# Performance work log

Measured on AMD Instinct MI355X. Metric: run time of the kernel, lower is better.

The kernel has to match this reference:

```python
import jax, jax.numpy as jnp
import numpy as np

LN_EPS = 1e-5

def layer_norm(x, w, b):
    m = jnp.mean(x, axis=-1, keepdims=True)
    v = jnp.mean((x - m) ** 2, axis=-1, keepdims=True)
    return (x - m) * jax.lax.rsqrt(v + LN_EPS) * w + b

def setup_inputs() -> dict:
    key = jax.random.key(0)
    ks = jax.random.split(key, 10)
    B, N, L = 32, 576, 100
    low, high = 1024, 1536
    inp = {
        "vit_feat": jax.random.normal(ks[0], (B, N, low), dtype=jnp.float32),
        "box_feat": jax.random.normal(ks[1], (B, L, high), dtype=jnp.float32),
        "lengths": jax.random.randint(ks[2], (B,), 0, L, dtype=jnp.int64),
        # query projector: LayerNorm(low) + Linear(low, low)
        "q_ln_w": jnp.ones((low,), jnp.float32),
        "q_ln_b": jnp.zeros((low,), jnp.float32),
        "q_w": jax.random.normal(ks[3], (low, low), dtype=jnp.float32) * 0.02,
        "q_b": jnp.zeros((low,), jnp.float32),
        # key projector: LayerNorm(high) + Linear(high, low)
        "k_ln_w": jnp.ones((high,), jnp.float32),
        "k_ln_b": jnp.zeros((high,), jnp.float32),
        "k_w": jax.random.normal(ks[4], (high, low), dtype=jnp.float32) * 0.02,
        "k_b": jnp.zeros((low,), jnp.float32),
        # value projector: LayerNorm(high) + Linear(high, low)
        "v_ln_w": jnp.ones((high,), jnp.float32),
        "v_ln_b": jnp.zeros((high,), jnp.float32),
        "v_w": jax.random.normal(ks[5], (high, low), dtype=jnp.float32) * 0.02,
        "v_b": jnp.zeros((low,), jnp.float32),
    }
    return inp

def reference(vit_feat, box_feat, lengths,
              q_ln_w, q_ln_b, q_w, q_b,
              k_ln_w, k_ln_b, k_w, k_b,
              v_ln_w, v_ln_b, v_w, v_b):
    B, L = box_feat.shape[0], box_feat.shape[1]
    # padding mask, same as the original per-row copy loop
    mask = jnp.arange(L)[None, :] < lengths[:, None]          # [B, L] bool
    q = layer_norm(vit_feat, q_ln_w, q_ln_b) @ q_w + q_b      # [B, N, low]
    k = layer_norm(box_feat, k_ln_w, k_ln_b) @ k_w + k_b      # [B, L, low]
    v = layer_norm(box_feat, v_ln_w, v_ln_b) @ v_w + v_b      # [B, L, low]
    scale = 1.0 / jnp.sqrt(jnp.asarray(k.shape[-1], q.dtype))
    att = jnp.einsum('bnd,bld->bnl', q, k * scale)            # [B, N, L]
    att = jnp.where(mask[:, None, :], att, -jnp.inf)
    att = jnp.nan_to_num(att)  # -inf -> finite min, matching torch nan_to_num
    att = jax.nn.softmax(att, axis=-1)
    out = jnp.einsum('bnl,bld->bnd', att, v)                  # [B, N, low]
    return vit_feat + out
```

## Files before the change

### kernel.cpp

```cpp
#include <hip/hip_runtime.h>
#include <stdint.h>

typedef __attribute__((ext_vector_type(8))) short short8;
typedef __attribute__((ext_vector_type(4))) float f32x4;

#define NEG_FLT_MAX (-3.402823466e38f)

__device__ __forceinline__ unsigned short f2bf(float f) {
  uint32_t u = __float_as_uint(f);
  uint32_t r = (u + 0x7fffu + ((u >> 16) & 1u)) >> 16;
  return (unsigned short)r;
}

__device__ __forceinline__ void gload16(const void* g, void* l) {
  __builtin_amdgcn_global_load_lds(
      (const __attribute__((address_space(1))) uint32_t*)g,
      (__attribute__((address_space(3))) uint32_t*)l, 16, 0, 0);
}

__device__ __forceinline__ void ln_vit_row(
    int row, const float* __restrict__ x, const float* __restrict__ w,
    const float* __restrict__ b, unsigned short* __restrict__ out, float* red) {
  const int t = threadIdx.x;
  const float4 v = ((const float4*)(x + (size_t)row * 1024))[t];
  float s = v.x + v.y + v.z + v.w;
  float ss = v.x * v.x + v.y * v.y + v.z * v.z + v.w * v.w;
#pragma unroll
  for (int off = 32; off > 0; off >>= 1) {
    s += __shfl_xor(s, off);
    ss += __shfl_xor(ss, off);
  }
  if ((t & 63) == 0) { red[(t >> 6) * 2] = s; red[(t >> 6) * 2 + 1] = ss; }
  __syncthreads();
  if (t == 0) {
    float a = 0.f, bb = 0.f;
    for (int i = 0; i < 4; i++) { a += red[i * 2]; bb += red[i * 2 + 1]; }
    red[0] = a; red[1] = bb;
  }
  __syncthreads();
  s = red[0]; ss = red[1];
  const float m = s * (1.f / 1024.f);
  const float var = ss * (1.f / 1024.f) - m * m;
  const float rstd = rsqrtf(var + 1e-5f);
  const float4 w4 = ((const float4*)w)[t];
  const float4 b4 = ((const float4*)b)[t];
  ushort4 o;
  o.x = f2bf((v.x - m) * rstd * w4.x + b4.x);
  o.y = f2bf((v.y - m) * rstd * w4.y + b4.y);
  o.z = f2bf((v.z - m) * rstd * w4.z + b4.z);
  o.w = f2bf((v.w - m) * rstd * w4.w + b4.w);
  ((ushort4*)(out + (size_t)row * 1024))[t] = o;
}

__device__ __forceinline__ void prep_body(
    int bid, const float* __restrict__ qw, const float* __restrict__ kw,
    const float* __restrict__ vw, const float* __restrict__ qb,
    const float* __restrict__ kb, float scale,
    unsigned short* __restrict__ qwb, unsigned short* __restrict__ kwb,
    unsigned short* __restrict__ vwt,
    float* __restrict__ bias3, float* __restrict__ w4, float* __restrict__ c4,
    float* tile ) {
  const int t = threadIdx.x;
  if (bid < 2560) {
    const int idx = bid * 256 + t;
    const int QG = 1024 * 1024 / 4;
    if (idx < QG) {
      float4 v = ((const float4*)qw)[idx];
      ushort4 o;
      o.x = f2bf(v.x); o.y = f2bf(v.y); o.z = f2bf(v.z); o.w = f2bf(v.w);
      ((ushort4*)qwb)[idx] = o;
    } else {
      const int j = idx - QG;
      float4 v = ((const float4*)kw)[j];
      ushort4 o;
      o.x = f2bf(v.x * scale); o.y = f2bf(v.y * scale);
      o.z = f2bf(v.z * scale); o.w = f2bf(v.w * scale);
      ((ushort4*)kwb)[j] = o;
    }
  } else if (bid < 4096) {
    const int j = bid - 2560;
    const int c0 = (j & 31) * 32, r0 = (j >> 5) * 32;
    const int tx = t & 31, ty = t >> 5;
#pragma unroll
    for (int i = ty; i < 32; i += 8)
      tile[i * 33 + tx] = vw[(size_t)(r0 + i) * 1024 + (c0 + tx)];
    __syncthreads();
#pragma unroll
    for (int i = ty; i < 32; i += 8)
      vwt[(size_t)(c0 + i) * 1536 + (r0 + tx)] = f2bf(tile[tx * 33 + i]);
  } else {
    const int idx = bid - 4096;
    const int wv = t >> 6, l = t & 63;
    float s = 0.f;
    if (idx < 256) {
      const int i = idx * 4 + wv;
      const float* row = qw + (size_t)i * 1024;
#pragma unroll
      for (int s0 = 0; s0 < 1024; s0 += 256) {
        float4 a = *(const float4*)(row + s0 + l * 4);
        float4 b = *(const float4*)(kb + s0 + l * 4);
        s += a.x * b.x + a.y * b.y + a.z * b.z + a.w * b.w;
      }
#pragma unroll
      for (int off = 32; off; off >>= 1) s += __shfl_xor(s, off);
      if (l == 0) bias3[i] = s * scale;
    } else if (idx < 640) {
      const int j = (idx - 256) * 4 + wv;
      const float* row = kw + (size_t)j * 1024;
#pragma unroll
      for (int s0 = 0; s0 < 1024; s0 += 256) {
        float4 a = *(const float4*)(row + s0 + l * 4);
        float4 b = *(const float4*)(qb + s0 + l * 4);
        s += a.x * b.x + a.y * b.y + a.z * b.z + a.w * b.w;
      }
#pragma unroll
      for (int off = 32; off; off >>= 1) s += __shfl_xor(s, off);
      if (l == 0) w4[j] = s * scale;
    } else if (wv == 0) {
#pragma unroll
      for (int s0 = 0; s0 < 1024; s0 += 256) {
        float4 a = *(const float4*)(qb + s0 + l * 4);
        float4 b = *(const float4*)(kb + s0 + l * 4);
        s += a.x * b.x + a.y * b.y + a.z * b.z + a.w * b.w;
      }
#pragma unroll
      for (int off = 32; off; off >>= 1) s += __shfl_xor(s, off);
      if (l == 0) *c4 = s * scale;
    }
  }
}

__global__ __launch_bounds__(256) void prep_kernel(
    const float* __restrict__ qw, const float* __restrict__ kw,
    const float* __restrict__ vw, const float* __restrict__ qb,
    const float* __restrict__ kb, float scale,
    unsigned short* __restrict__ qwb, unsigned short* __restrict__ kwb,
    unsigned short* __restrict__ vwt,
    float* __restrict__ bias3, float* __restrict__ w4, float* __restrict__ c4) {
  __shared__ float tile[32 * 33];
  prep_body(blockIdx.x, qw, kw, vw, qb, kb, scale, qwb, kwb, vwt,
            bias3, w4, c4, tile);
}

__global__ __launch_bounds__(256) void prepln_kernel(
    const float* __restrict__ qw, const float* __restrict__ kw,
    const float* __restrict__ vw, const float* __restrict__ qb,
    const float* __restrict__ kb, float scale,
    unsigned short* __restrict__ qwb, unsigned short* __restrict__ kwb,
    unsigned short* __restrict__ vwt,
    float* __restrict__ bias3, float* __restrict__ w4, float* __restrict__ c4,
    const float* __restrict__ vit, const float* __restrict__ qlnw,
    const float* __restrict__ qlnb, unsigned short* __restrict__ qn) {
  __shared__ float tile[32 * 33];
  __shared__ float red[8];
  const int bid = blockIdx.x;
  if (bid < 4737) {
    prep_body(bid, qw, kw, vw, qb, kb, scale, qwb, kwb, vwt,
              bias3, w4, c4, tile);
  } else {
    ln_vit_row(bid - 4737, vit, qlnw, qlnb, qn, red);
  }
}

__device__ __forceinline__ void gemm_core64(
    const unsigned short* __restrict__ A, int lda, int rowmaxA, int tm0,
    const unsigned short* __restrict__ Bt, int ldb, int rowmaxB, int tn0,
    int K, unsigned short* As, unsigned short* Bs, f32x4 acc[4][4]) {
  const int tid = threadIdx.x;
  const int w = tid >> 6, l = tid & 63;
  const int wr = w >> 1, wc = w & 1;
  const int srow = (w << 4) + (l >> 2);
  const int scol = (l & 3) << 3;
  int ra0 = tm0 + srow;      if (ra0 > rowmaxA) ra0 = rowmaxA;
  int ra1 = tm0 + srow + 64; if (ra1 > rowmaxA) ra1 = rowmaxA;
  int rb0 = tn0 + srow;      if (rb0 > rowmaxB) rb0 = rowmaxB;
  int rb1 = tn0 + srow + 64; if (rb1 > rowmaxB) rb1 = rowmaxB;
  const unsigned short* pa0 = A + (size_t)ra0 * lda + scol;
  const unsigned short* pa1 = A + (size_t)ra1 * lda + scol;
  const unsigned short* pb0 = Bt + (size_t)rb0 * ldb + scol;
  const unsigned short* pb1 = Bt + (size_t)rb1 * ldb + scol;
  unsigned short* la0 = As + (w << 4) * 32;
  unsigned short* la1 = As + ((w << 4) + 64) * 32;
  unsigned short* lb0 = Bs + (w << 4) * 32;
  unsigned short* lb1 = Bs + ((w << 4) + 64) * 32;
  const int foff = ((l & 15) << 5) + ((l >> 4) << 3);
  const unsigned short* fa = As + (wr << 6) * 32 + foff;
  const unsigned short* fb = Bs + (wc << 6) * 32 + foff;
#pragma unroll
  for (int i = 0; i < 4; i++)
#pragma unroll
    for (int j = 0; j < 4; j++) acc[i][j] = (f32x4)0.0f;
  for (int k0 = 0; k0 < K; k0 += 64) {
    gload16(pa0 + k0, la0);
    gload16(pa1 + k0, la1);
    gload16(pb0 + k0, lb0);
    gload16(pb1 + k0, lb1);
    gload16(pa0 + k0 + 32, la0 + 4096);
    gload16(pa1 + k0 + 32, la1 + 4096);
    gload16(pb0 + k0 + 32, lb0 + 4096);
    gload16(pb1 + k0 + 32, lb1 + 4096);
    __syncthreads();
    {
      short8 a[4], b[4];
#pragma unroll
      for (int i = 0; i < 4; i++) a[i] = *(const short8*)(fa + i * 512);
#pragma unroll
      for (int j = 0; j < 4; j++) b[j] = *(const short8*)(fb + j * 512);
#pragma unroll
      for (int i = 0; i < 4; i++)
#pragma unroll
        for (int j = 0; j < 4; j++)
          acc[i][j] = __builtin_amdgcn_mfma_f32_16x16x32_bf16(a[i], b[j], acc[i][j], 0, 0, 0);
    }
    {
      short8 a[4], b[4];
#pragma unroll
      for (int i = 0; i < 4; i++) a[i] = *(const short8*)(fa + 4096 + i * 512);
#pragma unroll
      for (int j = 0; j < 4; j++) b[j] = *(const short8*)(fb + 4096 + j * 512);
#pragma unroll
      for (int i = 0; i < 4; i++)
#pragma unroll
        for (int j = 0; j < 4; j++)
          acc[i][j] = __builtin_amdgcn_mfma_f32_16x16x32_bf16(a[i], b[j], acc[i][j], 0, 0, 0);
    }
    __syncthreads();
  }
}

__device__ __forceinline__ void gemm_core_db(
    const unsigned short* __restrict__ A, int lda, int rowmaxA, int tm0,
    const unsigned short* __restrict__ Bt, int ldb, int rowmaxB, int tn0,
    int K, unsigned short* As, unsigned short* Bs, f32x4 acc[4][4]) {
  const int tid = threadIdx.x;
  const int w = tid >> 6, l = tid & 63;
  const int wr = w >> 1, wc = w & 1;
  const int srow = (w << 4) + (l >> 2);
  const int scol = (l & 3) << 3;
  int ra0 = tm0 + srow;      if (ra0 > rowmaxA) ra0 = rowmaxA;
  int ra1 = tm0 + srow + 64; if (ra1 > rowmaxA) ra1 = rowmaxA;
  int rb0 = tn0 + srow;      if (rb0 > rowmaxB) rb0 = rowmaxB;
  int rb1 = tn0 + srow + 64; if (rb1 > rowmaxB) rb1 = rowmaxB;
  const unsigned short* pa0 = A + (size_t)ra0 * lda + scol;
  const unsigned short* pa1 = A + (size_t)ra1 * lda + scol;
  const unsigned short* pb0 = Bt + (size_t)rb0 * ldb + scol;
  const unsigned short* pb1 = Bt + (size_t)rb1 * ldb + scol;
  unsigned short* la0 = As + (w << 4) * 32;
  unsigned short* la1 = As + ((w << 4) + 64) * 32;
  unsigned short* lb0 = Bs + (w << 4) * 32;
  unsigned short* lb1 = Bs + ((w << 4) + 64) * 32;
  const int faoff = (wr << 6) * 32 + ((l & 15) << 5) + ((l >> 4) << 3);
  const int fboff = (wc << 6) * 32 + ((l & 15) << 5) + ((l >> 4) << 3);
#pragma unroll
  for (int i = 0; i < 4; i++)
#pragma unroll
    for (int j = 0; j < 4; j++) acc[i][j] = (f32x4)0.0f;

#define STAGE8(k0, bo) do {                                                  \
    gload16(pa0 + (k0), la0 + (bo));                                         \
    gload16(pa1 + (k0), la1 + (bo));                                         \
    gload16(pb0 + (k0), lb0 + (bo));                                         \
    gload16(pb1 + (k0), lb1 + (bo));                                         \
    gload16(pa0 + (k0) + 32, la0 + (bo) + 4096);                             \
    gload16(pa1 + (k0) + 32, la1 + (bo) + 4096);                             \
    gload16(pb0 + (k0) + 32, lb0 + (bo) + 4096);                             \
    gload16(pb1 + (k0) + 32, lb1 + (bo) + 4096);                             \
  } while (0)

  STAGE8(0, 0);
  __syncthreads();
  int p = 0;
  for (int k0 = 0; k0 < K; k0 += 64) {
    if (k0 + 64 < K) STAGE8(k0 + 64, (p ^ 1) * 8192);
    const unsigned short* fa = As + p * 8192 + faoff;
    const unsigned short* fb = Bs + p * 8192 + fboff;
    {
      short8 a[4], b[4];
#pragma unroll
      for (int i = 0; i < 4; i++) a[i] = *(const short8*)(fa + i * 512);
#pragma unroll
      for (int j = 0; j < 4; j++) b[j] = *(const short8*)(fb + j * 512);
#pragma unroll
      for (int i = 0; i < 4; i++)
#pragma unroll
        for (int j = 0; j < 4; j++)
          acc[i][j] = __builtin_amdgcn_mfma_f32_16x16x32_bf16(a[i], b[j], acc[i][j], 0, 0, 0);
    }
    {
      short8 a[4], b[4];
#pragma unroll
      for (int i = 0; i < 4; i++) a[i] = *(const short8*)(fa + 4096 + i * 512);
#pragma unroll
      for (int j = 0; j < 4; j++) b[j] = *(const short8*)(fb + 4096 + j * 512);
#pragma unroll
      for (int i = 0; i < 4; i++)
#pragma unroll
        for (int j = 0; j < 4; j++)
          acc[i][j] = __builtin_amdgcn_mfma_f32_16x16x32_bf16(a[i], b[j], acc[i][j], 0, 0, 0);
    }
    __syncthreads();
    p ^= 1;
  }
#undef STAGE8
}

__global__ __launch_bounds__(256) void mid_kernel(
    const float* __restrict__ box,
    const float* __restrict__ klnw, const float* __restrict__ klnb,
    const float* __restrict__ vlnw, const float* __restrict__ vlnb,
    const unsigned short* __restrict__ qwb, const unsigned short* __restrict__ kwb,
    const float* __restrict__ w4v, const float* __restrict__ c4,
    unsigned short* __restrict__ kn, unsigned short* __restrict__ vn,
    unsigned short* __restrict__ W3, float* __restrict__ qbk) {
  __shared__ float red[8];
  __shared__ float redq[4];
  __shared__ unsigned short As[128 * 64];
  __shared__ unsigned short Bs[128 * 64];
  const int t = threadIdx.x;
  if (blockIdx.x < 3200) {
    const int row = blockIdx.x;
    const float4* xr = (const float4*)(box + (size_t)row * 1536);
    const float4 a = xr[t];
    float4 c = make_float4(0.f, 0.f, 0.f, 0.f);
    if (t < 128) c = xr[256 + t];
    float s = a.x + a.y + a.z + a.w + c.x + c.y + c.z + c.w;
    float ss = a.x * a.x + a.y * a.y + a.z * a.z + a.w * a.w +
               c.x * c.x + c.y * c.y + c.z * c.z + c.w * c.w;
#pragma unroll
    for (int off = 32; off > 0; off >>= 1) {
      s += __shfl_xor(s, off);
      ss += __shfl_xor(ss, off);
    }
    if ((t & 63) == 0) { red[(t >> 6) * 2] = s; red[(t >> 6) * 2 + 1] = ss; }
    __syncthreads();
    if (t == 0) {
      float aa = 0.f, bb = 0.f;
      for (int i = 0; i < 4; i++) { aa += red[i * 2]; bb += red[i * 2 + 1]; }
      red[0] = aa; red[1] = bb;
    }
    __syncthreads();
    s = red[0]; ss = red[1];
    const float m = s * (1.f / 1536.f);
    const float var = ss * (1.f / 1536.f) - m * m;
    const float rstd = rsqrtf(var + 1e-5f);
    float qd;
    {
      const float4 w4 = ((const float4*)klnw)[t];
      const float4 b4 = ((const float4*)klnb)[t];
      const float k0v = (a.x - m) * rstd * w4.x + b4.x;
      const float k1v = (a.y - m) * rstd * w4.y + b4.y;
      const float k2v = (a.z - m) * rstd * w4.z + b4.z;
      const float k3v = (a.w - m) * rstd * w4.w + b4.w;
      ushort4 o;
      o.x = f2bf(k0v); o.y = f2bf(k1v); o.z = f2bf(k2v); o.w = f2bf(k3v);
      ((ushort4*)(kn + (size_t)row * 1536))[t] = o;
      const float4 wq = ((const float4*)w4v)[t];
      qd = k0v * wq.x + k1v * wq.y + k2v * wq.z + k3v * wq.w;
      const float4 w4vv = ((const float4*)vlnw)[t];
      const float4 b4vv = ((const float4*)vlnb)[t];
      o.x = f2bf((a.x - m) * rstd * w4vv.x + b4vv.x);
      o.y = f2bf((a.y - m) * rstd * w4vv.y + b4vv.y);
      o.z = f2bf((a.z - m) * rstd * w4vv.z + b4vv.z);
      o.w = f2bf((a.w - m) * rstd * w4vv.w + b4vv.w);
      ((ushort4*)(vn + (size_t)row * 1536))[t] = o;
    }
    if (t < 128) {
      const int t2 = 256 + t;
      const float4 w4 = ((const float4*)klnw)[t2];
      const float4 b4 = ((const float4*)klnb)[t2];
      const float k0v = (c.x - m) * rstd * w4.x + b4.x;
      const float k1v = (c.y - m) * rstd * w4.y + b4.y;
      const float k2v = (c.z - m) * rstd * w4.z + b4.z;
      const float k3v = (c.w - m) * rstd * w4.w + b4.w;
      ushort4 o;
      o.x = f2bf(k0v); o.y = f2bf(k1v); o.z = f2bf(k2v); o.w = f2bf(k3v);
      ((ushort4*)(kn + (size_t)row * 1536))[t2] = o;
      const float4 wq = ((const float4*)w4v)[t2];
      qd += k0v * wq.x + k1v * wq.y + k2v * wq.z + k3v * wq.w;
      const float4 w4vv = ((const float4*)vlnw)[t2];
      const float4 b4vv = ((const float4*)vlnb)[t2];
      o.x = f2bf((c.x - m) * rstd * w4vv.x + b4vv.x);
      o.y = f2bf((c.y - m) * rstd * w4vv.y + b4vv.y);
      o.z = f2bf((c.z - m) * rstd * w4vv.z + b4vv.z);
      o.w = f2bf((c.w - m) * rstd * w4vv.w + b4vv.w);
      ((ushort4*)(vn + (size_t)row * 1536))[t2] = o;
    }
#pragma unroll
    for (int off = 32; off; off >>= 1) qd += __shfl_xor(qd, off);
    if ((t & 63) == 0) redq[t >> 6] = qd;
    __syncthreads();
    if (t == 0) qbk[row] = redq[0] + redq[1] + redq[2] + redq[3] + c4[0];
  } else {
    const int j = blockIdx.x - 3200;
    const int tm0 = (j & 7) * 128, tn0 = (j >> 3) * 128;
    f32x4 acc[4][4];
    gemm_core64(qwb, 1024, 1023, tm0, kwb, 1024, 1535, tn0, 1024, As, Bs, acc);
    const int w = t >> 6, l = t & 63;
    const int wr = w >> 1, wc = w & 1;
#pragma unroll
    for (int i = 0; i < 4; i++) {
      const int row0 = tm0 + wr * 64 + i * 16 + (l >> 4) * 4;
#pragma unroll
      for (int jj = 0; jj < 4; jj++) {
        const int col = tn0 + wc * 64 + jj * 16 + (l & 15);
#pragma unroll
        for (int r = 0; r < 4; r++)
          W3[(size_t)(row0 + r) * 1536 + col] = f2bf(acc[i][jj][r]);
      }
    }
  }
}

__global__ __launch_bounds__(256) void gemm_kv_kernel(
    const unsigned short* __restrict__ kn, const unsigned short* __restrict__ vn,
    const unsigned short* __restrict__ W3, const unsigned short* __restrict__ vwt,
    const float* __restrict__ bias3, const float* __restrict__ vb,
    unsigned short* __restrict__ kq, unsigned short* __restrict__ vT) {
  extern __shared__ unsigned short lds[];
  unsigned short* As = lds;
  unsigned short* Bs = lds + 16384;
  const int id = blockIdx.x;
  const int sw = (id & 7) * 50 + (id >> 3);
  const int z = sw / 200;
  const int rem = sw - z * 200;
  const int tm0 = (rem % 25) * 128, tn0 = (rem / 25) * 128;
  const unsigned short* A = z ? vn : kn;
  const unsigned short* Bt = z ? vwt : W3;
  const float* bias = z ? vb : bias3;
  f32x4 acc[4][4];
  gemm_core_db(A, 1536, 3199, tm0, Bt, 1536, 1023, tn0, 1536, As, Bs, acc);
  const int tid = threadIdx.x;
  const int w = tid >> 6, l = tid & 63;
  const int wr = w >> 1, wc = w & 1;
#pragma unroll
  for (int i = 0; i < 4; i++) {
    const int row0 = tm0 + wr * 64 + i * 16 + (l >> 4) * 4;
#pragma unroll
    for (int j = 0; j < 4; j++) {
      const int col = tn0 + wc * 64 + j * 16 + (l & 15);
      const float bv = bias[col];
#pragma unroll
      for (int r = 0; r < 4; r++) {
        const int row = row0 + r;
        const float val = acc[i][j][r] + bv;
        if (!z) {
          kq[(size_t)row * 1024 + col] = f2bf(val);
        } else {
          const int bb = row / 100;
          const int ll = row - bb * 100;
          vT[((size_t)bb * 1024 + col) * 128 + ll] = f2bf(val);
        }
      }
    }
  }
}

__global__ __launch_bounds__(256) void ln_vit_kernel(
    const float* __restrict__ x, const float* __restrict__ w,
    const float* __restrict__ b, unsigned short* __restrict__ out) {
  __shared__ float red[8];
  ln_vit_row(blockIdx.x, x, w, b, out, red);
}

__global__ __launch_bounds__(256) void attfused_kernel(
    const unsigned short* __restrict__ qn, const unsigned short* __restrict__ kq,
    const unsigned short* __restrict__ vT, const float* __restrict__ qbk,
    const int* __restrict__ lengths, const float* __restrict__ vit,
    float* __restrict__ out) {
  __shared__ __align__(16) char smem[45824];
  float* Smat = (float*)smem;
  float* invr = (float*)(smem + 28672);
  float* qb_l = (float*)(smem + 28800);
  const int PB = 20480, BV = 29440;

  const int id = blockIdx.x;
  const int swz = (id & 7) * 72 + (id >> 3);
  const int b = swz / 18;
  const int tm0 = (swz - b * 18) * 32;
  const int t = threadIdx.x;
  const int w = t >> 6, l = t & 63;
  const int lo = l & 15, hi = l >> 4;
  if (t < 128) qb_l[t] = (t < 100) ? qbk[b * 100 + t] : 0.f;

  const unsigned short* A = qn + (size_t)b * 576 * 1024;
  const unsigned short* B = kq + (size_t)b * 100 * 1024;
  const int ar = (t & 127) >> 2, ah = t >> 7, ac = (t & 3) << 3;
  const unsigned short* paA = A + (size_t)(tm0 + ar) * 1024 + ah * 32 + ac;
  const unsigned short* pbB[4];
#pragma unroll
  for (int i = 0; i < 4; i++) {
    int rb = (i & 1) * 64 + (t >> 2); if (rb > 99) rb = 99;
    pbB[i] = B + (size_t)rb * 1024 + (i >> 1) * 32 + ((t & 3) << 3);
  }
  const int cw = w << 5;

  f32x4 acc[2][2];
#pragma unroll
  for (int i = 0; i < 2; i++) { acc[i][0] = (f32x4)0.0f; acc[i][1] = (f32x4)0.0f; }

  for (int k0 = 0; k0 < 1024; k0 += 64) {
    gload16(paA + k0, smem + w * 1024);
#pragma unroll
    for (int i = 0; i < 4; i++)
      gload16(pbB[i] + k0, smem + 4096 + i * 4096 + w * 1024);
    __syncthreads();
#pragma unroll
    for (int half = 0; half < 2; half++) {
      short8 a[2], bb[2];
#pragma unroll
      for (int i = 0; i < 2; i++)
        a[i] = *(const short8*)(smem + half * 2048 + (i * 16 + lo) * 64 + hi * 16);
#pragma unroll
      for (int j = 0; j < 2; j++)
        bb[j] = *(const short8*)(smem + 4096 + half * 8192 + (cw + j * 16 + lo) * 64 + hi * 16);
#pragma unroll
      for (int i = 0; i < 2; i++)
#pragma unroll
        for (int j = 0; j < 2; j++)
          acc[i][j] = __builtin_amdgcn_mfma_f32_16x16x32_bf16(a[i], bb[j], acc[i][j], 0, 0, 0);
    }
    __syncthreads();
  }

#pragma unroll
  for (int i = 0; i < 2; i++) {
    const int r0 = i * 16 + hi * 4;
#pragma unroll
    for (int j = 0; j < 2; j++) {
      const int c = cw + j * 16 + lo;
      const float qb = qb_l[c];
#pragma unroll
      for (int rr = 0; rr < 4; rr++) Smat[c * 36 + r0 + rr] = acc[i][j][rr] + qb;
    }
  }
  __syncthreads();

  const int r = t >> 3, g = t & 7;
  const int len = lengths[b];
  float mx = NEG_FLT_MAX;
#pragma unroll
  for (int i = 0; i < 13; i++) {
    const int ll = g * 13 + i;
    if (ll < 100) {
      const float v = (ll < len) ? Smat[ll * 36 + r] : NEG_FLT_MAX;
      mx = fmaxf(mx, v);
    }
  }
  mx = fmaxf(mx, __shfl_xor(mx, 1));
  mx = fmaxf(mx, __shfl_xor(mx, 2));
  mx = fmaxf(mx, __shfl_xor(mx, 4));
  float sum = 0.f;
#pragma unroll
  for (int i = 0; i < 13; i++) {
    const int ll = g * 13 + i;
    if (ll < 100) {
      const float v = (ll < len) ? Smat[ll * 36 + r] : NEG_FLT_MAX;
      const float e = __expf(v - mx);
      Smat[ll * 36 + r] = e;
      sum += e;
    }
  }
  sum += __shfl_xor(sum, 1);
  sum += __shfl_xor(sum, 2);
  sum += __shfl_xor(sum, 4);
  if (g == 0) invr[r] = 1.f / sum;
  __syncthreads();

  {
    const float inv = invr[r];
#pragma unroll
    for (int jj = 0; jj < 4; jj++) {
      const int c0 = g * 16 + jj * 4;
      ushort4 o;
      o.x = (c0 + 0 < 100) ? f2bf(Smat[(c0 + 0) * 36 + r] * inv) : (unsigned short)0;
      o.y = (c0 + 1 < 100) ? f2bf(Smat[(c0 + 1) * 36 + r] * inv) : (unsigned short)0;
      o.z = (c0 + 2 < 100) ? f2bf(Smat[(c0 + 2) * 36 + r] * inv) : (unsigned short)0;
      o.w = (c0 + 3 < 100) ? f2bf(Smat[(c0 + 3) * 36 + r] * inv) : (unsigned short)0;
      const int phys = (r * 256 + g * 32 + jj * 8) ^ ((r & 7) << 4);
      *(ushort4*)(smem + PB + phys) = o;
    }
  }
  __syncthreads();

  const unsigned short* vTb = vT + (size_t)b * 131072;
  const float* vitb = vit + ((size_t)b * 576 + tm0) * 1024;
  float* outb = out + ((size_t)b * 576 + tm0) * 1024;
  const int sBcol = ((t & 15) ^ ((t >> 4) & 7)) << 3;
  for (int nt = 0; nt < 16; ++nt) {
#pragma unroll
    for (int i = 0; i < 4; i++) {
      const int vrow = nt * 64 + i * 16 + (t >> 4);
      gload16(vTb + (size_t)vrow * 128 + sBcol, smem + BV + i * 4096 + w * 1024);
    }
    __syncthreads();
    f32x4 acc2[2];
    acc2[0] = (f32x4)0.0f; acc2[1] = (f32x4)0.0f;
#pragma unroll
    for (int ks = 0; ks < 4; ks++) {
      short8 av[2], bv;
#pragma unroll
      for (int i = 0; i < 2; i++) {
        const int m = i * 16 + lo;
        av[i] = *(const short8*)(smem + PB + ((m * 256 + ks * 64 + hi * 16) ^ ((m & 7) << 4)));
      }
      const int n = (w << 4) + lo;
      bv = *(const short8*)(smem + BV + ((n * 256 + ks * 64 + hi * 16) ^ ((n & 7) << 4)));
      acc2[0] = __builtin_amdgcn_mfma_f32_16x16x32_bf16(av[0], bv, acc2[0], 0, 0, 0);
      acc2[1] = __builtin_amdgcn_mfma_f32_16x16x32_bf16(av[1], bv, acc2[1], 0, 0, 0);
    }
#pragma unroll
    for (int i = 0; i < 2; i++) {
      const int col = (w << 4) + lo;
#pragma unroll
      for (int rr = 0; rr < 4; rr++) {
        const int row = i * 16 + hi * 4 + rr;
        *(float*)(smem + ((row * 256 + col * 4) ^ ((row & 7) << 4))) = acc2[i][rr];
      }
    }
    __syncthreads();
#pragma unroll
    for (int m = 0; m < 2; m++) {
      const int row = m * 16 + (t >> 4);
      const int colb = (t & 15) * 4;
      float4 e = *(const float4*)(smem + ((row * 256 + colb * 4) ^ ((row & 7) << 4)));
      const size_t gidx = (size_t)row * 1024 + nt * 64 + colb;
      float4 vv = *(const float4*)(vitb + gidx);
      e.x += vv.x; e.y += vv.y; e.z += vv.z; e.w += vv.w;
      *(float4*)(outb + gidx) = e;
    }
    __syncthreads();
  }
}

extern "C" void kernel_launch(void* const* d_in, const int* in_sizes, int n_in,
                              void* d_out, int out_size, void* d_ws, size_t ws_size,
                              hipStream_t stream) {
  const float* vit = (const float*)d_in[0];
  const float* box = (const float*)d_in[1];
  const int* lengths = (const int*)d_in[2];
  const float* q_ln_w = (const float*)d_in[3];
  const float* q_ln_b = (const float*)d_in[4];
  const float* q_w = (const float*)d_in[5];
  const float* q_b = (const float*)d_in[6];
  const float* k_ln_w = (const float*)d_in[7];
  const float* k_ln_b = (const float*)d_in[8];
  const float* k_w = (const float*)d_in[9];
  const float* k_b = (const float*)d_in[10];
  const float* v_ln_w = (const float*)d_in[11];
  const float* v_ln_b = (const float*)d_in[12];
  const float* v_w = (const float*)d_in[13];
  const float* v_b = (const float*)d_in[14];
  float* out = (float*)d_out;
  char* ws = (char*)d_ws;

  unsigned short* kn    = (unsigned short*)(ws + 0);
  unsigned short* vn    = (unsigned short*)(ws + 9830400);
  unsigned short* v_wt  = (unsigned short*)(ws + 19660800);
  unsigned short* qwb   = (unsigned short*)(ws + 22806528);
  unsigned short* kwb   = (unsigned short*)(ws + 24903680);
  unsigned short* W3    = (unsigned short*)(ws + 28049408);
  float*          bias3 = (float*)(ws + 31195136);
  float*          w4    = (float*)(ws + 31199232);
  float*          c4    = (float*)(ws + 31207424);
  float*          qbk   = (float*)(ws + 37748736);
  unsigned short* kq    = (unsigned short*)(ws + 37761536);
  unsigned short* vT    = (unsigned short*)(ws + 44315136);
  const bool merged = (ws_size >= 90452480ull);
  unsigned short* qn = merged ? (unsigned short*)(ws + 52703744)
                              : (unsigned short*)(ws + 0);

  const float scale = 0.03125f;

  (void)hipFuncSetAttribute((const void*)gemm_kv_kernel,
                            hipFuncAttributeMaxDynamicSharedMemorySize, 65536);

  if (merged) {
    prepln_kernel<<<23169, 256, 0, stream>>>(
        q_w, k_w, v_w, q_b, k_b, scale, qwb, kwb, v_wt, bias3, w4, c4,
        vit, q_ln_w, q_ln_b, qn);
    mid_kernel<<<3296, 256, 0, stream>>>(box, k_ln_w, k_ln_b, v_ln_w, v_ln_b,
                                         qwb, kwb, w4, c4, kn, vn, W3, qbk);
    gemm_kv_kernel<<<400, 256, 65536, stream>>>(kn, vn, W3, v_wt, bias3, v_b, kq, vT);
    attfused_kernel<<<576, 256, 0, stream>>>(qn, kq, vT, qbk, lengths, vit, out);
  } else {
    prep_kernel<<<4737, 256, 0, stream>>>(q_w, k_w, v_w, q_b, k_b, scale,
                                          qwb, kwb, v_wt, bias3, w4, c4);
    mid_kernel<<<3296, 256, 0, stream>>>(box, k_ln_w, k_ln_b, v_ln_w, v_ln_b,
                                         qwb, kwb, w4, c4, kn, vn, W3, qbk);
    gemm_kv_kernel<<<400, 256, 65536, stream>>>(kn, vn, W3, v_wt, bias3, v_b, kq, vT);
    ln_vit_kernel<<<18432, 256, 0, stream>>>(vit, q_ln_w, q_ln_b, qn);
    attfused_kernel<<<576, 256, 0, stream>>>(qn, kq, vT, qbk, lengths, vit, out);
  }

  (void)in_sizes; (void)n_in; (void)out_size;
}
```

Measured before the change: 143.3 us.

## Split-K the K/V projection GEMM into two halves with a combine pass

Adds a split-K variant of the K/V projection GEMM that launches 800 blocks instead of 400, so more CUs are busy on the 256-CU part. Each half covers 768 of the 1536 reduction dimension and writes bf16 partials to separate workspace buffers. A combine kernel then adds the partials and the biases. The cost is an extra launch, extra memory traffic, and an added bf16 rounding of the partial sums. It is only taken when the workspace is large enough.

```diff
diff --git a/kernel.cpp b/kernel.cpp
--- a/kernel.cpp
+++ b/kernel.cpp
@@ -10,6 +10,10 @@
   uint32_t u = __float_as_uint(f);
   uint32_t r = (u + 0x7fffu + ((u >> 16) & 1u)) >> 16;
   return (unsigned short)r;
+}
+
+__device__ __forceinline__ float bf2f(unsigned short u) {
+  return __uint_as_float(((uint32_t)u) << 16);
 }
 
 __device__ __forceinline__ void gload16(const void* g, void* l) {
@@ -455,6 +459,92 @@
   }
 }
 
+__global__ __launch_bounds__(256) void gemm_kv_split_kernel(
+    const unsigned short* __restrict__ kn, const unsigned short* __restrict__ vn,
+    const unsigned short* __restrict__ W3, const unsigned short* __restrict__ vwt,
+    unsigned short* __restrict__ kq, unsigned short* __restrict__ vT,
+    unsigned short* __restrict__ kqp1, unsigned short* __restrict__ vTp1) {
+  extern __shared__ unsigned short lds[];
+  unsigned short* As = lds;
+  unsigned short* Bs = lds + 16384;
+  const int id = blockIdx.x;
+  const int sw = (id & 7) * 100 + (id >> 3);
+  const int split = sw / 400;
+  const int rest = sw - split * 400;
+  const int z = rest / 200;
+  const int rem = rest - z * 200;
+  const int tm0 = (rem % 25) * 128, tn0 = (rem / 25) * 128;
+  const unsigned short* A = (z ? vn : kn) + split * 768;
+  const unsigned short* Bt = (z ? vwt : W3) + split * 768;
+  f32x4 acc[4][4];
+  gemm_core_db(A, 1536, 3199, tm0, Bt, 1536, 1023, tn0, 768, As, Bs, acc);
+  unsigned short* kdst = split ? kqp1 : kq;
+  unsigned short* vdst = split ? vTp1 : vT;
+  const int tid = threadIdx.x;
+  const int w = tid >> 6, l = tid & 63;
+  const int wr = w >> 1, wc = w & 1;
+#pragma unroll
+  for (int i = 0; i < 4; i++) {
+    const int row0 = tm0 + wr * 64 + i * 16 + (l >> 4) * 4;
+#pragma unroll
+    for (int j = 0; j < 4; j++) {
+      const int col = tn0 + wc * 64 + j * 16 + (l & 15);
+#pragma unroll
+      for (int r = 0; r < 4; r++) {
+        const int row = row0 + r;
+        const float val = acc[i][j][r];
+        if (!z) {
+          kdst[(size_t)row * 1024 + col] = f2bf(val);
+        } else {
+          const int bb = row / 100;
+          const int ll = row - bb * 100;
+          vdst[((size_t)bb * 1024 + col) * 128 + ll] = f2bf(val);
+        }
+      }
+    }
+  }
+}
+
+__global__ __launch_bounds__(256) void combine_kernel(
+    unsigned short* __restrict__ kq, const unsigned short* __restrict__ kqp1,
+    unsigned short* __restrict__ vT, const unsigned short* __restrict__ vTp1,
+    const float* __restrict__ bias3, const float* __restrict__ vb) {
+  const int t = threadIdx.x;
+  const int bid = blockIdx.x;
+  if (bid < 800) {
+    const size_t base = (size_t)bid * 4096 + t * 16;
+    const int col0 = (int)(base & 1023);
+    short8 a0 = *(const short8*)(kq + base);
+    short8 a1 = *(const short8*)(kq + base + 8);
+    short8 b0 = *(const short8*)(kqp1 + base);
+    short8 b1 = *(const short8*)(kqp1 + base + 8);
+    short8 o0, o1;
+#pragma unroll
+    for (int j = 0; j < 8; j++) {
+      o0[j] = (short)f2bf(bf2f((unsigned short)a0[j]) + bf2f((unsigned short)b0[j]) + bias3[col0 + j]);
+      o1[j] = (short)f2bf(bf2f((unsigned short)a1[j]) + bf2f((unsigned short)b1[j]) + bias3[col0 + 8 + j]);
+    }
+    *(short8*)(kq + base) = o0;
+    *(short8*)(kq + base + 8) = o1;
+  } else {
+    const size_t base = (size_t)(bid - 800) * 4096 + t * 16;
+    const int col = (int)((base >> 7) & 1023);
+    const float bv = vb[col];
+    short8 a0 = *(const short8*)(vT + base);
+    short8 a1 = *(const short8*)(vT + base + 8);
+    short8 b0 = *(const short8*)(vTp1 + base);
+    short8 b1 = *(const short8*)(vTp1 + base + 8);
+    short8 o0, o1;
+#pragma unroll
+    for (int j = 0; j < 8; j++) {
+      o0[j] = (short)f2bf(bf2f((unsigned short)a0[j]) + bf2f((unsigned short)b0[j]) + bv);
+      o1[j] = (short)f2bf(bf2f((unsigned short)a1[j]) + bf2f((unsigned short)b1[j]) + bv);
+    }
+    *(short8*)(vT + base) = o0;
+    *(short8*)(vT + base + 8) = o1;
+  }
+}
+
 __global__ __launch_bounds__(256) void ln_vit_kernel(
     const float* __restrict__ x, const float* __restrict__ w,
     const float* __restrict__ b, unsigned short* __restrict__ out) {
@@ -666,12 +756,17 @@
   unsigned short* kq    = (unsigned short*)(ws + 37761536);
   unsigned short* vT    = (unsigned short*)(ws + 44315136);
   const bool merged = (ws_size >= 90452480ull);
-  unsigned short* qn = merged ? (unsigned short*)(ws + 52703744)
-                              : (unsigned short*)(ws + 0);
+  const bool ksplit = (ws_size >= 105394688ull);
+  unsigned short* qn   = merged ? (unsigned short*)(ws + 52703744)
+                                : (unsigned short*)(ws + 0);
+  unsigned short* kqp1 = (unsigned short*)(ws + 90452480);
+  unsigned short* vTp1 = (unsigned short*)(ws + 97006080);
 
   const float scale = 0.03125f;
 
   (void)hipFuncSetAttribute((const void*)gemm_kv_kernel,
+                            hipFuncAttributeMaxDynamicSharedMemorySize, 65536);
+  (void)hipFuncSetAttribute((const void*)gemm_kv_split_kernel,
                             hipFuncAttributeMaxDynamicSharedMemorySize, 65536);
 
   if (merged) {
@@ -680,7 +775,13 @@
         vit, q_ln_w, q_ln_b, qn);
     mid_kernel<<<3296, 256, 0, stream>>>(box, k_ln_w, k_ln_b, v_ln_w, v_ln_b,
                                          qwb, kwb, w4, c4, kn, vn, W3, qbk);
-    gemm_kv_kernel<<<400, 256, 65536, stream>>>(kn, vn, W3, v_wt, bias3, v_b, kq, vT);
+    if (ksplit) {
+      gemm_kv_split_kernel<<<800, 256, 65536, stream>>>(
+          kn, vn, W3, v_wt, kq, vT, kqp1, vTp1);
+      combine_kernel<<<1824, 256, 0, stream>>>(kq, kqp1, vT, vTp1, bias3, v_b);
+    } else {
+      gemm_kv_kernel<<<400, 256, 65536, stream>>>(kn, vn, W3, v_wt, bias3, v_b, kq, vT);
+    }
     attfused_kernel<<<576, 256, 0, stream>>>(qn, kq, vT, qbk, lengths, vit, out);
   } else {
     prep_kernel<<<4737, 256, 0, stream>>>(q_w, k_w, v_w, q_b, k_b, scale,
```

Result: slower. 164.9 us (+15.0%).
